# Kernel tuning notes

Hardware: AMD Instinct MI355X
Metric: run time of the kernel (lower is better)

## Reference

```python
import jax, jax.numpy as jnp
import numpy as np
import math

FEATURE_DIM = 128
CLASS_NUM = 10000
BATCH = 4096


def setup_inputs() -> dict:
    key = jax.random.key(0)
    k1, k2, k3 = jax.random.split(key, 3)
    # feat scaled by 0.1 so squared distances are O(1) and exp(-d/1.8) is non-degenerate
    feat = jax.random.normal(k1, (BATCH, FEATURE_DIM), dtype=jnp.float32) * 0.1
    # xavier_uniform over [class_num, feature_dim]
    bound = math.sqrt(6.0 / (CLASS_NUM + FEATURE_DIM))
    weights = jax.random.uniform(k2, (CLASS_NUM, FEATURE_DIM), dtype=jnp.float32,
                                 minval=-bound, maxval=bound)
    label = jax.random.randint(k3, (BATCH,), 0, CLASS_NUM, dtype=jnp.int64)
    return {"feat": feat, "weights": weights, "label": label}


def reference(feat, weights, label):
    # pairwise squared euclidean distance via GEMM trick (avoids [B,C,D] diff tensor)
    f2 = jnp.sum(feat * feat, axis=-1, keepdims=True)          # [B,1]
    w2 = jnp.sum(weights * weights, axis=-1)[None, :]          # [1,C]
    metric = jnp.maximum(f2 + w2 - 2.0 * (feat @ weights.T), 0.0)  # [B,C]
    kernal_metric = jnp.exp(-metric / 1.8)                     # [B,C]
    # per-sample gather of the true-class kernel value; mean; clamp at 0.5
    cor = jnp.take_along_axis(kernal_metric, label[:, None].astype(jnp.int32), axis=1)[:, 0]
    avg = jnp.maximum(jnp.mean(cor), 0.5)
    # original uses .item() per sample -> scale is detached from the graph
    scale = jax.lax.stop_gradient(1.0 / avg) * math.log(CLASS_NUM - 1.0)
    return scale * kernal_metric
```

## Files before the change

kernel.cpp:

```cpp
#include <hip/hip_runtime.h>
#include <hip/hip_bf16.h>
#include <math.h>

#define FDIM  128
#define BATCH 4096
#define CNUM  10000

typedef __attribute__((ext_vector_type(8))) short short8;
typedef __attribute__((ext_vector_type(4))) float f32x4;

#define WS_FEATB 0
#define WS_WB    1048576
#define WS_F2    3608576
#define WS_W2    3624960
#define WS_COR   3664960
#define WS_LS2   3681344

#define C2 0.80178372573096f

#define GL2LDS(g, l) __builtin_amdgcn_global_load_lds(                      \
    (const __attribute__((address_space(1))) void*)(g),                     \
    (__attribute__((address_space(3))) void*)(l), 16, 0, 0)

__global__ void prep_cor_kernel(const float* __restrict__ feat,
                                const float* __restrict__ weights,
                                const int* __restrict__ label,
                                __hip_bfloat16* __restrict__ featb,
                                __hip_bfloat16* __restrict__ wb,
                                float* __restrict__ f2,
                                float* __restrict__ w2,
                                float* __restrict__ cor) {
    int gw   = (blockIdx.x * blockDim.x + threadIdx.x) >> 6;
    int lane = threadIdx.x & 63;
    if (gw < BATCH + CNUM) {
        const float* src;
        __hip_bfloat16* dst;
        float* nrm;
        if (gw < BATCH) { src = feat    + (size_t)gw * FDIM; dst = featb + (size_t)gw * FDIM; nrm = f2 + gw; }
        else            { int r = gw - BATCH;
                          src = weights + (size_t)r  * FDIM; dst = wb    + (size_t)r  * FDIM; nrm = w2 + r; }
        float2 v = ((const float2*)src)[lane];
        __hip_bfloat162 b2;
        b2.x = __float2bfloat16(v.x);
        b2.y = __float2bfloat16(v.y);
        ((__hip_bfloat162*)dst)[lane] = b2;
        float ss = v.x * v.x + v.y * v.y;
        #pragma unroll
        for (int off = 32; off; off >>= 1) ss += __shfl_down(ss, off, 64);
        if (lane == 0) *nrm = ss;
    } else {
        int s = gw - (BATCH + CNUM);
        if (s >= BATCH) return;
        int lab = label[s];
        float2 f = ((const float2*)(feat    + (size_t)s   * FDIM))[lane];
        float2 w = ((const float2*)(weights + (size_t)lab * FDIM))[lane];
        float dx = f.x - w.x, dy = f.y - w.y;
        float ss = dx * dx + dy * dy;
        #pragma unroll
        for (int off = 32; off; off >>= 1) ss += __shfl_down(ss, off, 64);
        if (lane == 0) cor[s] = __expf(-ss * (1.0f / 1.8f));
    }
}

__global__ void scale_kernel(const float* __restrict__ cor, float* __restrict__ ls2) {
    __shared__ float red[4];
    int t = threadIdx.x;
    float s = 0.0f;
    #pragma unroll
    for (int i = 0; i < BATCH / 256; i++) s += cor[t + i * 256];
    #pragma unroll
    for (int off = 32; off; off >>= 1) s += __shfl_down(s, off, 64);
    if ((t & 63) == 0) red[t >> 6] = s;
    __syncthreads();
    if (t == 0) {
        float avg = (red[0] + red[1] + red[2] + red[3]) * (1.0f / BATCH);
        avg = fmaxf(avg, 0.5f);
        *ls2 = log2f(logf((float)(CNUM - 1)) / avg);
    }
}

__launch_bounds__(512, 4)
__global__ void gemm_kernel(const __hip_bfloat16* __restrict__ featb,
                            const __hip_bfloat16* __restrict__ wb,
                            const float* __restrict__ f2,
                            const float* __restrict__ w2,
                            const float* __restrict__ ls2_p,
                            float* __restrict__ out) {
    __shared__ __align__(16) char lds[65536];

    int bx   = blockIdx.x;
    int band = bx & 31;
    int cg   = bx >> 5;
    int tid  = threadIdx.x;
    int wid  = tid >> 6;
    int lane = tid & 63;
    int r16  = lane & 15;
    int kh   = lane >> 4;
    int aoff = (wid & 1) * 64;
    int boff = (wid >> 1) * 32;
    int t0   = cg * 5;

    const char* Ab = (const char*)wb;
    const char* Bb = (const char*)featb;

    #pragma unroll
    for (int p = 0; p < 4; ++p) {
        int idx = tid + p * 512;
        int row = idx >> 4, chk = idx & 15;
        int grow = band * 128 + row;
        GL2LDS(Bb + (size_t)grow * 256 + (chk ^ (row & 7)) * 16, lds + 32768 + idx * 16);
    }
    #pragma unroll
    for (int p = 0; p < 4; ++p) {
        int idx = tid + p * 512;
        int row = idx >> 4, chk = idx & 15;
        int gc = t0 * 128 + row; gc = gc < CNUM ? gc : CNUM - 1;
        GL2LDS(Ab + (size_t)gc * 256 + (chk ^ (row & 7)) * 16, lds + idx * 16);
    }
    float ls2 = *ls2_p;
    float f2n[2];
    #pragma unroll
    for (int n = 0; n < 2; ++n) f2n[n] = f2[band * 128 + boff + n * 16 + r16];
    __syncthreads();

    short8 bfrag[4][2];
    #pragma unroll
    for (int kk = 0; kk < 4; ++kk)
        #pragma unroll
        for (int n = 0; n < 2; ++n) {
            int row = boff + n * 16 + r16;
            int c = (kk * 4 + kh) ^ (row & 7);
            bfrag[kk][n] = *(const short8*)(lds + 32768 + row * 256 + c * 16);
        }
    __syncthreads();

    #pragma unroll
    for (int it = 0; it < 5; ++it) {
        int t = t0 + it;
        int cur = it & 1;

        if (it < 4) {
            #pragma unroll
            for (int p = 0; p < 4; ++p) {
                int idx = tid + p * 512;
                int row = idx >> 4, chk = idx & 15;
                int gc = (t + 1) * 128 + row; gc = gc < CNUM ? gc : CNUM - 1;
                GL2LDS(Ab + (size_t)gc * 256 + (chk ^ (row & 7)) * 16,
                       lds + (cur ^ 1) * 32768 + idx * 16);
            }
        }

        const char* Abuf = lds + cur * 32768;
        f32x4 acc[4][2];
        #pragma unroll
        for (int m = 0; m < 4; ++m)
            #pragma unroll
            for (int n = 0; n < 2; ++n) acc[m][n] = (f32x4){0.f, 0.f, 0.f, 0.f};

        #pragma unroll
        for (int kk = 0; kk < 4; ++kk) {
            short8 a[4];
            #pragma unroll
            for (int m = 0; m < 4; ++m) {
                int row = aoff + m * 16 + r16;
                int c = (kk * 4 + kh) ^ (row & 7);
                a[m] = *(const short8*)(Abuf + row * 256 + c * 16);
            }
            #pragma unroll
            for (int m = 0; m < 4; ++m)
                #pragma unroll
                for (int n = 0; n < 2; ++n)
                    acc[m][n] = __builtin_amdgcn_mfma_f32_16x16x32_bf16(a[m], bfrag[kk][n], acc[m][n], 0, 0, 0);
        }

        int mbase = t * 128 + aoff;
        #pragma unroll
        for (int m = 0; m < 4; ++m) {
            int cm0 = mbase + m * 16 + kh * 4;
            bool ok = cm0 < CNUM;
            f32x4 w4 = *(const f32x4*)(w2 + (ok ? cm0 : 0));
            #pragma unroll
            for (int n = 0; n < 2; ++n) {
                f32x4 v;
                #pragma unroll
                for (int r = 0; r < 4; ++r) {
                    float mt2 = fmaf(-2.0f, acc[m][n][r], f2n[n] + w4[r]);
                    mt2 = fmaxf(mt2, 0.0f);
                    v[r] = exp2f(fmaf(mt2, -C2, ls2));
                }
                if (ok) {
                    size_t rg = (size_t)(band * 128 + boff + n * 16 + r16);
                    *(f32x4*)(out + rg * CNUM + cm0) = v;
                }
            }
        }

        asm volatile("s_waitcnt vmcnt(12)" ::: "memory");
        __builtin_amdgcn_sched_barrier(0);
        __builtin_amdgcn_s_barrier();
    }
}

extern "C" void kernel_launch(void* const* d_in, const int* in_sizes, int n_in,
                              void* d_out, int out_size, void* d_ws, size_t ws_size,
                              hipStream_t stream) {
    (void)in_sizes; (void)n_in; (void)out_size; (void)ws_size;
    const float* feat    = (const float*)d_in[0];
    const float* weights = (const float*)d_in[1];
    const int*   label   = (const int*)d_in[2];
    float* out = (float*)d_out;
    char*  ws  = (char*)d_ws;

    __hip_bfloat16* featb = (__hip_bfloat16*)(ws + WS_FEATB);
    __hip_bfloat16* wb    = (__hip_bfloat16*)(ws + WS_WB);
    float* f2  = (float*)(ws + WS_F2);
    float* w2  = (float*)(ws + WS_W2);
    float* cor = (float*)(ws + WS_COR);
    float* ls2 = (float*)(ws + WS_LS2);

    const int total_waves = BATCH + CNUM + BATCH;
    prep_cor_kernel<<<(total_waves + 3) / 4, 256, 0, stream>>>(
        feat, weights, label, featb, wb, f2, w2, cor);
    scale_kernel<<<1, 256, 0, stream>>>(cor, ls2);

    gemm_kernel<<<512, 512, 0, stream>>>(featb, wb, f2, w2, ls2, out);
}
```

Measured before the change: 49.68 us.

## Fuse scale reduction into GEMM, load feature fragments directly, interleave class tiles

```diff
diff --git a/kernel.cpp b/kernel.cpp
--- a/kernel.cpp
+++ b/kernel.cpp
@@ -14,7 +14,6 @@
 #define WS_F2    3608576
 #define WS_W2    3624960
 #define WS_COR   3664960
-#define WS_LS2   3681344
 
 #define C2 0.80178372573096f
 
@@ -62,31 +61,15 @@
     }
 }
 
-__global__ void scale_kernel(const float* __restrict__ cor, float* __restrict__ ls2) {
-    __shared__ float red[4];
-    int t = threadIdx.x;
-    float s = 0.0f;
-    #pragma unroll
-    for (int i = 0; i < BATCH / 256; i++) s += cor[t + i * 256];
-    #pragma unroll
-    for (int off = 32; off; off >>= 1) s += __shfl_down(s, off, 64);
-    if ((t & 63) == 0) red[t >> 6] = s;
-    __syncthreads();
-    if (t == 0) {
-        float avg = (red[0] + red[1] + red[2] + red[3]) * (1.0f / BATCH);
-        avg = fmaxf(avg, 0.5f);
-        *ls2 = log2f(logf((float)(CNUM - 1)) / avg);
-    }
-}
-
 __launch_bounds__(512, 4)
 __global__ void gemm_kernel(const __hip_bfloat16* __restrict__ featb,
                             const __hip_bfloat16* __restrict__ wb,
                             const float* __restrict__ f2,
                             const float* __restrict__ w2,
-                            const float* __restrict__ ls2_p,
+                            const float* __restrict__ cor,
                             float* __restrict__ out) {
     __shared__ __align__(16) char lds[65536];
+    __shared__ float red[8];
 
     int bx   = blockIdx.x;
     int band = bx & 31;
@@ -98,57 +81,65 @@
     int kh   = lane >> 4;
     int aoff = (wid & 1) * 64;
     int boff = (wid >> 1) * 32;
-    int t0   = cg * 5;
 
     const char* Ab = (const char*)wb;
-    const char* Bb = (const char*)featb;
 
     #pragma unroll
     for (int p = 0; p < 4; ++p) {
         int idx = tid + p * 512;
         int row = idx >> 4, chk = idx & 15;
-        int grow = band * 128 + row;
-        GL2LDS(Bb + (size_t)grow * 256 + (chk ^ (row & 7)) * 16, lds + 32768 + idx * 16);
-    }
-    #pragma unroll
-    for (int p = 0; p < 4; ++p) {
-        int idx = tid + p * 512;
-        int row = idx >> 4, chk = idx & 15;
-        int gc = t0 * 128 + row; gc = gc < CNUM ? gc : CNUM - 1;
+        int gc = cg * 128 + row; gc = gc < CNUM ? gc : CNUM - 1;
         GL2LDS(Ab + (size_t)gc * 256 + (chk ^ (row & 7)) * 16, lds + idx * 16);
     }
-    float ls2 = *ls2_p;
+
+    {
+        float s = 0.0f;
+        #pragma unroll
+        for (int i = 0; i < BATCH / 512; ++i) s += cor[tid + i * 512];
+        #pragma unroll
+        for (int off = 32; off; off >>= 1) s += __shfl_down(s, off, 64);
+        if (lane == 0) red[wid] = s;
+    }
+
     float f2n[2];
     #pragma unroll
     for (int n = 0; n < 2; ++n) f2n[n] = f2[band * 128 + boff + n * 16 + r16];
+
     __syncthreads();
 
+    float tot = 0.0f;
+    #pragma unroll
+    for (int i = 0; i < 8; ++i) tot += red[i];
+    float avg = fmaxf(tot * (1.0f / BATCH), 0.5f);
+    float ls2 = log2f(logf((float)(CNUM - 1)) / avg);
+
+    const char* Bb = (const char*)featb;
     short8 bfrag[4][2];
     #pragma unroll
     for (int kk = 0; kk < 4; ++kk)
         #pragma unroll
         for (int n = 0; n < 2; ++n) {
-            int row = boff + n * 16 + r16;
-            int c = (kk * 4 + kh) ^ (row & 7);
-            bfrag[kk][n] = *(const short8*)(lds + 32768 + row * 256 + c * 16);
-        }
-    __syncthreads();
+            int row = band * 128 + boff + n * 16 + r16;
+            bfrag[kk][n] = *(const short8*)(Bb + (size_t)row * 256 + kk * 64 + kh * 16);
+        }
 
     #pragma unroll
     for (int it = 0; it < 5; ++it) {
-        int t = t0 + it;
+        int t   = it * 16 + cg;
         int cur = it & 1;
 
         if (it < 4) {
+            int tn = t + 16;
             #pragma unroll
             for (int p = 0; p < 4; ++p) {
                 int idx = tid + p * 512;
                 int row = idx >> 4, chk = idx & 15;
-                int gc = (t + 1) * 128 + row; gc = gc < CNUM ? gc : CNUM - 1;
+                int gc = tn * 128 + row; gc = gc < CNUM ? gc : CNUM - 1;
                 GL2LDS(Ab + (size_t)gc * 256 + (chk ^ (row & 7)) * 16,
                        lds + (cur ^ 1) * 32768 + idx * 16);
             }
         }
+        __builtin_amdgcn_sched_barrier(0);
 
         const char* Abuf = lds + cur * 32768;
         f32x4 acc[4][2];
@@ -195,7 +186,7 @@
             }
         }
 
-        asm volatile("s_waitcnt vmcnt(12)" ::: "memory");
+        asm volatile("s_waitcnt vmcnt(8)" ::: "memory");
         __builtin_amdgcn_sched_barrier(0);
         __builtin_amdgcn_s_barrier();
     }
@@ -216,12 +207,10 @@
     float* f2  = (float*)(ws + WS_F2);
     float* w2  = (float*)(ws + WS_W2);
     float* cor = (float*)(ws + WS_COR);
-    float* ls2 = (float*)(ws + WS_LS2);
 
     const int total_waves = BATCH + CNUM + BATCH;
     prep_cor_kernel<<<(total_waves + 3) / 4, 256, 0, stream>>>(
         feat, weights, label, featb, wb, f2, w2, cor);
-    scale_kernel<<<1, 256, 0, stream>>>(cor, ls2);
-
-    gemm_kernel<<<512, 512, 0, stream>>>(featb, wb, f2, w2, ls2, out);
+
+    gemm_kernel<<<512, 512, 0, stream>>>(featb, wb, f2, w2, cor, out);
 }
```

Result: no change. 49.60 us (-0.2%).
